# Performance work log

Hardware: AMD Instinct MI355X
Metric: run time of the kernel (lower is better)

## Reference

```python
import jax, jax.numpy as jnp
import numpy as np

NY, NU, NH = 64, 64, 256  # Nhidden=256 -> 128 complex eigen pairs
T, NB = 4096, 32          # horizon, batch


def setup_inputs() -> dict:
    key = jax.random.key(0)
    ks = jax.random.split(key, 9)
    return {
        "y0": jax.random.normal(ks[0], (NB, NY), jnp.float32),
        "U": jax.random.normal(ks[1], (T, NB, NU), jnp.float32),
        "lmbd_cont_real": jax.random.uniform(ks[2], (NH // 2,), jnp.float32),
        "lmbd_cont_imag": jax.random.uniform(ks[3], (NH // 2,), jnp.float32),
        "B": jax.random.normal(ks[4], (NH, NU), jnp.float32) / np.sqrt(NU),
        "W_y2x": jax.random.normal(ks[5], (NH, NY), jnp.float32) / np.sqrt(NY),
        "b_y2x": jax.random.normal(ks[6], (NH,), jnp.float32) * 0.01,
        "W_x2y": jax.random.normal(ks[7], (NY, NH), jnp.float32) / np.sqrt(NH),
        "b_x2y": jax.random.normal(ks[8], (NY,), jnp.float32) * 0.01,
    }


def reference(y0, U, lmbd_cont_real, lmbd_cont_imag, B, W_y2x, b_y2x, W_x2y, b_x2y):
    # where A is the real 2x2-block form of complex eigenvalues
    # lambda = r * exp(i*theta), r = exp(-|re|), theta = (pi/2)*im.
    # Original builds A^n explicitly (O(T^2)); an O(T) scan computes the same math.
    H = B.shape[0] // 2
    Bu = jnp.einsum('tbu,hu->tbh', U, B)          # (T, NB, NH)
    r = jnp.exp(-jnp.abs(lmbd_cont_real))
    theta = (jnp.pi / 2) * lmbd_cont_imag
    lr = r * jnp.cos(theta)                        # Re(lambda), (H,)
    li = r * jnp.sin(theta)                        # Im(lambda), (H,)
    x0 = y0 @ W_y2x.T + b_y2x                      # (NB, NH)
    zr0, zi0 = x0[:, :H], x0[:, H:]
    a, b = Bu[:, :, :H], Bu[:, :, H:]

    def step(carry, inp):
        zr, zi = carry
        ak, bk = inp
        nzr = lr * zr - li * zi + ak
        nzi = li * zr + lr * zi + bk
        return (nzr, nzi), (nzr, nzi)

    _, (Xr, Xi) = jax.lax.scan(step, (zr0, zi0), (a, b))
    X = jnp.concatenate([Xr, Xi], axis=-1)         # (T, NB, NH)
    Y = X @ W_x2y.T + b_x2y                        # (T, NB, NY)
    return Y
```

## Files before the change

kernel.cpp:

```cpp
#include <hip/hip_runtime.h>
#include <math.h>

#define TT   4096
#define NBB  32
#define NUU  64
#define NHH  256
#define HH   128
#define NYY  64
#define LCH  8
#define CCH  512
#define SEGN 16
#define CPS  32

#define PI_HALF 1.5707963267948966f

typedef float  f32x16 __attribute__((ext_vector_type(16)));
typedef __bf16 bf16x8 __attribute__((ext_vector_type(8)));
typedef __bf16 bf16x2 __attribute__((ext_vector_type(2)));
typedef unsigned int uint4v __attribute__((ext_vector_type(4)));

__device__ inline int crow(int r, int lane) { return (r & 3) + 8 * (r >> 2) + 4 * (lane >> 5); }
__device__ inline bf16x8 ldfrag(const unsigned short* p) {
    return __builtin_bit_cast(bf16x8, *(const uint4v*)p);
}

#define CVT(v, H, L) { __bf16 _h = (__bf16)(v); H = _h; L = (__bf16)((v) - (float)_h); }

__device__ inline void lam_f32(float xre, float xim, float& lr, float& li) {
    float th = PI_HALF * xim;
    float rf = (float)exp(-(double)fabsf(xre));
    float cf = (float)cos((double)th);
    float sf = (float)sin((double)th);
    lr = rf * cf; li = rf * sf;
}

__device__ inline int swzU(int row, int so) {
    return row * 128 + ((((so >> 3) ^ row) & 15) << 3) + (so & 7);
}
__device__ inline int swzX(int row, int so) {
    int chv = so >> 3;
    chv = (chv & 32) | ((chv ^ row) & 31);
    return row * 512 + (chv << 3) + (so & 7);
}

__global__ __launch_bounds__(256) void k_prep(
    const float* __restrict__ B, const float* __restrict__ W,
    const float* __restrict__ y0, const float* __restrict__ Wy2x,
    const float* __restrict__ by2x,
    unsigned short* __restrict__ Bph, unsigned short* __restrict__ Bpl,
    unsigned short* __restrict__ Wph, unsigned short* __restrict__ Wpl,
    float2* __restrict__ x0p)
{
    int bx = blockIdx.x, tid = threadIdx.x;
    if (bx < 32) {
        if (tid < HH) {
            int b = bx, ch = tid;
            float xr = by2x[ch], xi = by2x[ch + HH];
            for (int y = 0; y < NYY; ++y) {
                float v = y0[b * NYY + y];
                xr += v * Wy2x[ch * NYY + y];
                xi += v * Wy2x[(ch + HH) * NYY + y];
            }
            x0p[b * HH + ch] = make_float2(xr, xi);
        }
    } else {
        int i = (bx - 32) * 256 + tid;
        float bv = B[i];
        __bf16 bh = (__bf16)bv;
        Bph[i] = __builtin_bit_cast(unsigned short, bh);
        Bpl[i] = __builtin_bit_cast(unsigned short, (__bf16)(bv - (float)bh));
        int y = i >> 8, kidx = i & 255;
        float wv = W[y * NHH + (kidx & 1) * HH + (kidx >> 1)];
        __bf16 wh = (__bf16)wv;
        Wph[i] = __builtin_bit_cast(unsigned short, wh);
        Wpl[i] = __builtin_bit_cast(unsigned short, (__bf16)(wv - (float)wh));
    }
}

__global__ __launch_bounds__(256, 1) void k_pass1(
    const float* __restrict__ U,
    const unsigned short* __restrict__ Bph, const unsigned short* __restrict__ Bpl,
    const float* __restrict__ lre, const float* __restrict__ lim,
    float2* __restrict__ E)
{
    __shared__ __align__(16) unsigned short sU[2][64 * 136];

    const int tid = threadIdx.x, w = tid >> 6, lane = tid & 63;
    const int l31 = lane & 31, kh = lane >> 5;
    const int c = blockIdx.x;
    const int ch = w * 32 + l31;

    float lr, li; lam_f32(lre[ch], lim[ch], lr, li);

    bf16x8 bfh[2][4], bfl[2][4];
#pragma unroll
    for (int nt = 0; nt < 2; ++nt)
#pragma unroll
        for (int kk = 0; kk < 4; ++kk) {
            bfh[nt][kk] = ldfrag(&Bph[(size_t)(nt * HH + ch) * NUU + kk * 16 + kh * 8]);
            bfl[nt][kk] = ldfrag(&Bpl[(size_t)(nt * HH + ch) * NUU + kk * 16 + kh * 8]);
        }

    float zr[16], zi[16];
#pragma unroll
    for (int r = 0; r < 16; ++r) { zr[r] = 0.f; zi[r] = 0.f; }

    const int srow = tid >> 2, sus = (tid & 3) * 16;
    const int sb = srow & 31, stoff = srow >> 5;
    const float* ubase = U + (size_t)sb * NUU + sus;

    float4 f0, f1, f2, f3;
    {
        const float4* sp = (const float4*)(ubase + (size_t)(c * LCH + stoff) * (NBB * NUU));
        f0 = sp[0]; f1 = sp[1]; f2 = sp[2]; f3 = sp[3];
    }

    for (int sub = 0; sub < 4; ++sub) {
        unsigned short* su = &sU[sub & 1][0];
        {
            bf16x8 h0, h1, l0, l1;
            CVT(f0.x, h0[0], l0[0]); CVT(f0.y, h0[1], l0[1]); CVT(f0.z, h0[2], l0[2]); CVT(f0.w, h0[3], l0[3]);
            CVT(f1.x, h0[4], l0[4]); CVT(f1.y, h0[5], l0[5]); CVT(f1.z, h0[6], l0[6]); CVT(f1.w, h0[7], l0[7]);
            CVT(f2.x, h1[0], l1[0]); CVT(f2.y, h1[1], l1[1]); CVT(f2.z, h1[2], l1[2]); CVT(f2.w, h1[3], l1[3]);
            CVT(f3.x, h1[4], l1[4]); CVT(f3.y, h1[5], l1[5]); CVT(f3.z, h1[6], l1[6]); CVT(f3.w, h1[7], l1[7]);
            *(bf16x8*)&su[srow * 136 + sus]          = h0;
            *(bf16x8*)&su[srow * 136 + sus + 8]      = h1;
            *(bf16x8*)&su[srow * 136 + 64 + sus]     = l0;
            *(bf16x8*)&su[srow * 136 + 64 + sus + 8] = l1;
        }
        __syncthreads();

        if (sub < 3) {
            const float4* sp = (const float4*)(ubase + (size_t)(c * LCH + (sub + 1) * 2 + stoff) * (NBB * NUU));
            f0 = sp[0]; f1 = sp[1]; f2 = sp[2]; f3 = sp[3];
        }

        f32x16 acc[2][2];
#pragma unroll
        for (int mt = 0; mt < 2; ++mt)
#pragma unroll
            for (int nt = 0; nt < 2; ++nt)
#pragma unroll
                for (int r = 0; r < 16; ++r) acc[mt][nt][r] = 0.f;

#pragma unroll
        for (int kk = 0; kk < 4; ++kk) {
            bf16x8 a0h = ldfrag(&su[(l31)      * 136 + kk * 16 + kh * 8]);
            bf16x8 a1h = ldfrag(&su[(32 + l31) * 136 + kk * 16 + kh * 8]);
            bf16x8 a0l = ldfrag(&su[(l31)      * 136 + 64 + kk * 16 + kh * 8]);
            bf16x8 a1l = ldfrag(&su[(32 + l31) * 136 + 64 + kk * 16 + kh * 8]);
            acc[0][0] = __builtin_amdgcn_mfma_f32_32x32x16_bf16(a0h, bfh[0][kk], acc[0][0], 0, 0, 0);
            acc[0][1] = __builtin_amdgcn_mfma_f32_32x32x16_bf16(a0h, bfh[1][kk], acc[0][1], 0, 0, 0);
            acc[1][0] = __builtin_amdgcn_mfma_f32_32x32x16_bf16(a1h, bfh[0][kk], acc[1][0], 0, 0, 0);
            acc[1][1] = __builtin_amdgcn_mfma_f32_32x32x16_bf16(a1h, bfh[1][kk], acc[1][1], 0, 0, 0);
            acc[0][0] = __builtin_amdgcn_mfma_f32_32x32x16_bf16(a0l, bfh[0][kk], acc[0][0], 0, 0, 0);
            acc[0][1] = __builtin_amdgcn_mfma_f32_32x32x16_bf16(a0l, bfh[1][kk], acc[0][1], 0, 0, 0);
            acc[1][0] = __builtin_amdgcn_mfma_f32_32x32x16_bf16(a1l, bfh[0][kk], acc[1][0], 0, 0, 0);
            acc[1][1] = __builtin_amdgcn_mfma_f32_32x32x16_bf16(a1l, bfh[1][kk], acc[1][1], 0, 0, 0);
            acc[0][0] = __builtin_amdgcn_mfma_f32_32x32x16_bf16(a0h, bfl[0][kk], acc[0][0], 0, 0, 0);
            acc[0][1] = __builtin_amdgcn_mfma_f32_32x32x16_bf16(a0h, bfl[1][kk], acc[0][1], 0, 0, 0);
            acc[1][0] = __builtin_amdgcn_mfma_f32_32x32x16_bf16(a1h, bfl[0][kk], acc[1][0], 0, 0, 0);
            acc[1][1] = __builtin_amdgcn_mfma_f32_32x32x16_bf16(a1h, bfl[1][kk], acc[1][1], 0, 0, 0);
        }

#pragma unroll
        for (int mt = 0; mt < 2; ++mt)
#pragma unroll
            for (int r = 0; r < 16; ++r) {
                float t0 = fmaf(lr, zr[r], acc[mt][0][r]); t0 = fmaf(-li, zi[r], t0);
                float t1 = fmaf(li, zr[r], acc[mt][1][r]); t1 = fmaf(lr, zi[r], t1);
                zr[r] = t0; zi[r] = t1;
            }
    }

#pragma unroll
    for (int r = 0; r < 16; ++r)
        E[(size_t)c * 4096 + crow(r, lane) * HH + ch] = make_float2(zr[r], zi[r]);
}

__global__ __launch_bounds__(256) void k_cseg(
    const float* __restrict__ lre, const float* __restrict__ lim,
    const float2* __restrict__ E, float2* __restrict__ Esup)
{
    int g = blockIdx.x * 256 + threadIdx.x;
    int chain = g & 4095, seg = g >> 12, ch = chain & 127;
    float lrf, lif; lam_f32(lre[ch], lim[ch], lrf, lif);
    double pr = (double)lrf, pi = (double)lif;
#pragma unroll
    for (int s = 0; s < 3; ++s) { double nr = pr*pr - pi*pi, ni = 2.0*pr*pi; pr = nr; pi = ni; }
    double sr = 0.0, si = 0.0;
#pragma unroll 8
    for (int j = 0; j < CPS; ++j) {
        float2 e = E[((size_t)seg * CPS + j) * 4096 + chain];
        double nr = pr * sr - pi * si + (double)e.x;
        double ni = pi * sr + pr * si + (double)e.y;
        sr = nr; si = ni;
    }
    Esup[(size_t)seg * 4096 + chain] = make_float2((float)sr, (float)si);
}

__global__ __launch_bounds__(256) void k_csup(
    const float* __restrict__ lre, const float* __restrict__ lim,
    const float2* __restrict__ x0p, const float2* __restrict__ Esup,
    float2* __restrict__ CarrySup)
{
    int chain = blockIdx.x * 256 + threadIdx.x;
    int ch = chain & 127;
    float lrf, lif; lam_f32(lre[ch], lim[ch], lrf, lif);
    double pr = (double)lrf, pi = (double)lif;
#pragma unroll
    for (int s = 0; s < 8; ++s) { double nr = pr*pr - pi*pi, ni = 2.0*pr*pi; pr = nr; pi = ni; }
    float2 c0 = x0p[chain];
    double cr = (double)c0.x, ci = (double)c0.y;
#pragma unroll
    for (int s = 0; s < SEGN; ++s) {
        CarrySup[(size_t)s * 4096 + chain] = make_float2((float)cr, (float)ci);
        float2 e = Esup[(size_t)s * 4096 + chain];
        double nr = pr * cr - pi * ci + (double)e.x;
        double ni = pi * cr + pr * ci + (double)e.y;
        cr = nr; ci = ni;
    }
}

__global__ __launch_bounds__(256) void k_cexp(
    const float* __restrict__ lre, const float* __restrict__ lim,
    const float2* __restrict__ E, const float2* __restrict__ CarrySup,
    float2* __restrict__ Carry)
{
    int g = blockIdx.x * 256 + threadIdx.x;
    int chain = g & 4095, seg = g >> 12, ch = chain & 127;
    float lrf, lif; lam_f32(lre[ch], lim[ch], lrf, lif);
    double pr = (double)lrf, pi = (double)lif;
#pragma unroll
    for (int s = 0; s < 3; ++s) { double nr = pr*pr - pi*pi, ni = 2.0*pr*pi; pr = nr; pi = ni; }
    float2 cc = CarrySup[(size_t)seg * 4096 + chain];
    double cr = (double)cc.x, ci = (double)cc.y;
#pragma unroll 8
    for (int j = 0; j < CPS; ++j) {
        size_t idx = ((size_t)seg * CPS + j) * 4096 + chain;
        Carry[idx] = make_float2((float)cr, (float)ci);
        float2 e = E[idx];
        double nr = pr * cr - pi * ci + (double)e.x;
        double ni = pi * cr + pr * ci + (double)e.y;
        cr = nr; ci = ni;
    }
}

__global__ __launch_bounds__(256, 1) void k_pass2(
    const float* __restrict__ U,
    const unsigned short* __restrict__ Bph, const unsigned short* __restrict__ Bpl,
    const unsigned short* __restrict__ Wph, const unsigned short* __restrict__ Wpl,
    const float* __restrict__ lre, const float* __restrict__ lim,
    const float* __restrict__ bx2y,
    const float2* __restrict__ Carry, float* __restrict__ Y)
{
    __shared__ __align__(16) unsigned short sU[64 * 128];
    __shared__ __align__(16) unsigned short sX[64 * 512];

    const int tid = threadIdx.x, w = tid >> 6, lane = tid & 63;
    const int l31 = lane & 31, kh = lane >> 5;
    const int c = blockIdx.x;
    const int ch = w * 32 + l31;
    const int mtile = w & 1, ntile = w >> 1;

    float lr, li; lam_f32(lre[ch], lim[ch], lr, li);
    float ybias = bx2y[ntile * 32 + l31];

    bf16x8 bfh[2][4], bfl[2][4];
#pragma unroll
    for (int nt = 0; nt < 2; ++nt)
#pragma unroll
        for (int kk = 0; kk < 4; ++kk) {
            bfh[nt][kk] = ldfrag(&Bph[(size_t)(nt * HH + ch) * NUU + kk * 16 + kh * 8]);
            bfl[nt][kk] = ldfrag(&Bpl[(size_t)(nt * HH + ch) * NUU + kk * 16 + kh * 8]);
        }

    bf16x8 wfh[16], wfl[16];
#pragma unroll
    for (int kk = 0; kk < 16; ++kk) {
        wfh[kk] = ldfrag(&Wph[(size_t)(ntile * 32 + l31) * NHH + kk * 16 + kh * 8]);
        wfl[kk] = ldfrag(&Wpl[(size_t)(ntile * 32 + l31) * NHH + kk * 16 + kh * 8]);
    }

    float zr[16], zi[16];
#pragma unroll
    for (int r = 0; r < 16; ++r) {
        float2 v = Carry[(size_t)c * 4096 + crow(r, lane) * HH + ch];
        zr[r] = v.x; zi[r] = v.y;
    }

    const int srow = tid >> 2, sus = (tid & 3) * 16;
    const int sb = srow & 31, stoff = srow >> 5;
    const float* ubase = U + (size_t)sb * NUU + sus;

    float4 f0, f1, f2, f3;
    {
        const float4* sp = (const float4*)(ubase + (size_t)(c * LCH + stoff) * (NBB * NUU));
        f0 = sp[0]; f1 = sp[1]; f2 = sp[2]; f3 = sp[3];
    }

    for (int sub = 0; sub < 4; ++sub) {
        {
            bf16x8 h0, h1, l0, l1;
            CVT(f0.x, h0[0], l0[0]); CVT(f0.y, h0[1], l0[1]); CVT(f0.z, h0[2], l0[2]); CVT(f0.w, h0[3], l0[3]);
            CVT(f1.x, h0[4], l0[4]); CVT(f1.y, h0[5], l0[5]); CVT(f1.z, h0[6], l0[6]); CVT(f1.w, h0[7], l0[7]);
            CVT(f2.x, h1[0], l1[0]); CVT(f2.y, h1[1], l1[1]); CVT(f2.z, h1[2], l1[2]); CVT(f2.w, h1[3], l1[3]);
            CVT(f3.x, h1[4], l1[4]); CVT(f3.y, h1[5], l1[5]); CVT(f3.z, h1[6], l1[6]); CVT(f3.w, h1[7], l1[7]);
            *(bf16x8*)&sU[swzU(srow, sus)]          = h0;
            *(bf16x8*)&sU[swzU(srow, sus + 8)]      = h1;
            *(bf16x8*)&sU[swzU(srow, 64 + sus)]     = l0;
            *(bf16x8*)&sU[swzU(srow, 64 + sus + 8)] = l1;
        }

        if (sub > 0) {
            f32x16 ya0, ya1, ya2;
#pragma unroll
            for (int r = 0; r < 16; ++r) { ya0[r] = 0.f; ya1[r] = 0.f; ya2[r] = 0.f; }
#pragma unroll
            for (int kk = 0; kk < 16; ++kk) {
                bf16x8 xah = ldfrag(&sX[swzX(mtile * 32 + l31, kk * 16 + kh * 8)]);
                bf16x8 xal = ldfrag(&sX[swzX(mtile * 32 + l31, 256 + kk * 16 + kh * 8)]);
                ya0 = __builtin_amdgcn_mfma_f32_32x32x16_bf16(xah, wfh[kk], ya0, 0, 0, 0);
                ya1 = __builtin_amdgcn_mfma_f32_32x32x16_bf16(xal, wfh[kk], ya1, 0, 0, 0);
                ya2 = __builtin_amdgcn_mfma_f32_32x32x16_bf16(xah, wfl[kk], ya2, 0, 0, 0);
            }
            int t = c * LCH + (sub - 1) * 2 + mtile;
#pragma unroll
            for (int r = 0; r < 16; ++r)
                Y[((size_t)t * NBB + crow(r, lane)) * NYY + ntile * 32 + l31] =
                    (ya0[r] + ya1[r]) + ya2[r] + ybias;
        }
        __syncthreads();

        if (sub < 3) {
            const float4* sp = (const float4*)(ubase + (size_t)(c * LCH + (sub + 1) * 2 + stoff) * (NBB * NUU));
            f0 = sp[0]; f1 = sp[1]; f2 = sp[2]; f3 = sp[3];
        }

        f32x16 acc[2][2];
#pragma unroll
        for (int mt = 0; mt < 2; ++mt)
#pragma unroll
            for (int nt = 0; nt < 2; ++nt)
#pragma unroll
                for (int r = 0; r < 16; ++r) acc[mt][nt][r] = 0.f;

#pragma unroll
        for (int kk = 0; kk < 4; ++kk) {
            bf16x8 a0h = ldfrag(&sU[swzU(l31,      kk * 16 + kh * 8)]);
            bf16x8 a1h = ldfrag(&sU[swzU(32 + l31, kk * 16 + kh * 8)]);
            bf16x8 a0l = ldfrag(&sU[swzU(l31,      64 + kk * 16 + kh * 8)]);
            bf16x8 a1l = ldfrag(&sU[swzU(32 + l31, 64 + kk * 16 + kh * 8)]);
            acc[0][0] = __builtin_amdgcn_mfma_f32_32x32x16_bf16(a0h, bfh[0][kk], acc[0][0], 0, 0, 0);
            acc[0][1] = __builtin_amdgcn_mfma_f32_32x32x16_bf16(a0h, bfh[1][kk], acc[0][1], 0, 0, 0);
            acc[1][0] = __builtin_amdgcn_mfma_f32_32x32x16_bf16(a1h, bfh[0][kk], acc[1][0], 0, 0, 0);
            acc[1][1] = __builtin_amdgcn_mfma_f32_32x32x16_bf16(a1h, bfh[1][kk], acc[1][1], 0, 0, 0);
            acc[0][0] = __builtin_amdgcn_mfma_f32_32x32x16_bf16(a0l, bfh[0][kk], acc[0][0], 0, 0, 0);
            acc[0][1] = __builtin_amdgcn_mfma_f32_32x32x16_bf16(a0l, bfh[1][kk], acc[0][1], 0, 0, 0);
            acc[1][0] = __builtin_amdgcn_mfma_f32_32x32x16_bf16(a1l, bfh[0][kk], acc[1][0], 0, 0, 0);
            acc[1][1] = __builtin_amdgcn_mfma_f32_32x32x16_bf16(a1l, bfh[1][kk], acc[1][1], 0, 0, 0);
            acc[0][0] = __builtin_amdgcn_mfma_f32_32x32x16_bf16(a0h, bfl[0][kk], acc[0][0], 0, 0, 0);
            acc[0][1] = __builtin_amdgcn_mfma_f32_32x32x16_bf16(a0h, bfl[1][kk], acc[0][1], 0, 0, 0);
            acc[1][0] = __builtin_amdgcn_mfma_f32_32x32x16_bf16(a1h, bfl[0][kk], acc[1][0], 0, 0, 0);
            acc[1][1] = __builtin_amdgcn_mfma_f32_32x32x16_bf16(a1h, bfl[1][kk], acc[1][1], 0, 0, 0);
        }

#pragma unroll
        for (int mt = 0; mt < 2; ++mt)
#pragma unroll
            for (int r = 0; r < 16; ++r) {
                float t0 = fmaf(lr, zr[r], acc[mt][0][r]); t0 = fmaf(-li, zi[r], t0);
                float t1 = fmaf(li, zr[r], acc[mt][1][r]); t1 = fmaf(lr, zi[r], t1);
                zr[r] = t0; zi[r] = t1;
                bf16x2 hv, lv;
                { __bf16 _h = (__bf16)t0; hv[0] = _h; lv[0] = (__bf16)(t0 - (float)_h); }
                { __bf16 _h = (__bf16)t1; hv[1] = _h; lv[1] = (__bf16)(t1 - (float)_h); }
                int row = mt * 32 + crow(r, lane);
                *(bf16x2*)&sX[swzX(row, w * 64 + 2 * l31)]       = hv;
                *(bf16x2*)&sX[swzX(row, 256 + w * 64 + 2 * l31)] = lv;
            }
        __syncthreads();
    }

    {
        f32x16 ya0, ya1, ya2;
#pragma unroll
        for (int r = 0; r < 16; ++r) { ya0[r] = 0.f; ya1[r] = 0.f; ya2[r] = 0.f; }
#pragma unroll
        for (int kk = 0; kk < 16; ++kk) {
            bf16x8 xah = ldfrag(&sX[swzX(mtile * 32 + l31, kk * 16 + kh * 8)]);
            bf16x8 xal = ldfrag(&sX[swzX(mtile * 32 + l31, 256 + kk * 16 + kh * 8)]);
            ya0 = __builtin_amdgcn_mfma_f32_32x32x16_bf16(xah, wfh[kk], ya0, 0, 0, 0);
            ya1 = __builtin_amdgcn_mfma_f32_32x32x16_bf16(xal, wfh[kk], ya1, 0, 0, 0);
            ya2 = __builtin_amdgcn_mfma_f32_32x32x16_bf16(xah, wfl[kk], ya2, 0, 0, 0);
        }
        int t = c * LCH + 3 * 2 + mtile;
#pragma unroll
        for (int r = 0; r < 16; ++r)
            Y[((size_t)t * NBB + crow(r, lane)) * NYY + ntile * 32 + l31] =
                (ya0[r] + ya1[r]) + ya2[r] + ybias;
    }
}

extern "C" void kernel_launch(void* const* d_in, const int* in_sizes, int n_in,
                              void* d_out, int out_size, void* d_ws, size_t ws_size,
                              hipStream_t stream) {
    const float* y0    = (const float*)d_in[0];
    const float* U     = (const float*)d_in[1];
    const float* lre   = (const float*)d_in[2];
    const float* lim   = (const float*)d_in[3];
    const float* B     = (const float*)d_in[4];
    const float* W_y2x = (const float*)d_in[5];
    const float* b_y2x = (const float*)d_in[6];
    const float* W_x2y = (const float*)d_in[7];
    const float* b_x2y = (const float*)d_in[8];
    float* Y = (float*)d_out;

    char* p = (char*)d_ws;
    float2* E        = (float2*)p; p += (size_t)CCH * 4096 * sizeof(float2);
    float2* Carry    = (float2*)p; p += (size_t)CCH * 4096 * sizeof(float2);
    float2* Esup     = (float2*)p; p += (size_t)SEGN * 4096 * sizeof(float2);
    float2* CarrySup = (float2*)p; p += (size_t)SEGN * 4096 * sizeof(float2);
    float2* x0p      = (float2*)p; p += (size_t)4096 * sizeof(float2);
    unsigned short* Bph = (unsigned short*)p; p += 16384 * sizeof(unsigned short);
    unsigned short* Bpl = (unsigned short*)p; p += 16384 * sizeof(unsigned short);
    unsigned short* Wph = (unsigned short*)p; p += 16384 * sizeof(unsigned short);
    unsigned short* Wpl = (unsigned short*)p; p += 16384 * sizeof(unsigned short);

    k_prep <<<dim3(96),  dim3(256), 0, stream>>>(B, W_x2y, y0, W_y2x, b_y2x, Bph, Bpl, Wph, Wpl, x0p);
    k_pass1<<<dim3(CCH), dim3(256), 0, stream>>>(U, Bph, Bpl, lre, lim, E);
    k_cseg <<<dim3(256), dim3(256), 0, stream>>>(lre, lim, E, Esup);
    k_csup <<<dim3(16),  dim3(256), 0, stream>>>(lre, lim, x0p, Esup, CarrySup);
    k_cexp <<<dim3(256), dim3(256), 0, stream>>>(lre, lim, E, CarrySup, Carry);
    k_pass2<<<dim3(CCH), dim3(256), 0, stream>>>(U, Bph, Bpl, Wph, Wpl, lre, lim, b_x2y, Carry, Y);
}
```

Measured before the change: 172.9 us.

## Fold chunk recurrence into lambda-power-weighted B and pre-split U to bf16

Pass1 now folds the 8-step within-chunk recurrence into a single K=512 GEMM, using a B matrix pre-weighted by powers of lambda that is built in the prep kernel. U is converted once to bf16 hi/lo arrays in the prep kernel. Pass1 and pass2 then read MFMA fragments straight from global memory instead of converting and staging through shared memory. This removes the serial recurrence and the repeated fp32-to-bf16 conversion, but adds an extra full write and reread of U (about 32MB of bf16 hi/lo) and a much larger prep grid.

```diff
diff --git a/kernel.cpp b/kernel.cpp
--- a/kernel.cpp
+++ b/kernel.cpp
@@ -34,9 +34,6 @@
     lr = rf * cf; li = rf * sf;
 }
 
-__device__ inline int swzU(int row, int so) {
-    return row * 128 + ((((so >> 3) ^ row) & 15) << 3) + (so & 7);
-}
 __device__ inline int swzX(int row, int so) {
     int chv = so >> 3;
     chv = (chv & 32) | ((chv ^ row) & 31);
@@ -47,8 +44,12 @@
     const float* __restrict__ B, const float* __restrict__ W,
     const float* __restrict__ y0, const float* __restrict__ Wy2x,
     const float* __restrict__ by2x,
+    const float* __restrict__ lre, const float* __restrict__ lim,
+    const float* __restrict__ U,
     unsigned short* __restrict__ Bph, unsigned short* __restrict__ Bpl,
     unsigned short* __restrict__ Wph, unsigned short* __restrict__ Wpl,
+    unsigned short* __restrict__ Bqh, unsigned short* __restrict__ Bql,
+    unsigned short* __restrict__ Uh,  unsigned short* __restrict__ Ul,
     float2* __restrict__ x0p)
 {
     int bx = blockIdx.x, tid = threadIdx.x;
@@ -63,7 +64,7 @@
             }
             x0p[b * HH + ch] = make_float2(xr, xi);
         }
-    } else {
+    } else if (bx < 96) {
         int i = (bx - 32) * 256 + tid;
         float bv = B[i];
         __bf16 bh = (__bf16)bv;
@@ -74,108 +75,81 @@
         __bf16 wh = (__bf16)wv;
         Wph[i] = __builtin_bit_cast(unsigned short, wh);
         Wpl[i] = __builtin_bit_cast(unsigned short, (__bf16)(wv - (float)wh));
-    }
-}
-
-__global__ __launch_bounds__(256, 1) void k_pass1(
-    const float* __restrict__ U,
-    const unsigned short* __restrict__ Bph, const unsigned short* __restrict__ Bpl,
-    const float* __restrict__ lre, const float* __restrict__ lim,
+    } else if (bx < 160) {
+        int e = (bx - 96) * 2048 + tid * 8;
+        int row = e >> 9, col = e & 511;
+        int j = col >> 6, u = col & 63;
+        int ch = (row < HH) ? row : (row - HH);
+        float lrf, lif; lam_f32(lre[ch], lim[ch], lrf, lif);
+        double pr = 1.0, pi_ = 0.0;
+        for (int s = 0; s < 7 - j; ++s) {
+            double nr = pr * (double)lrf - pi_ * (double)lif;
+            double ni = pr * (double)lif + pi_ * (double)lrf;
+            pr = nr; pi_ = ni;
+        }
+        for (int k = 0; k < 8; ++k) {
+            double b0 = (double)B[ch * NUU + u + k];
+            double b1 = (double)B[(ch + HH) * NUU + u + k];
+            float val = (row < HH) ? (float)(pr * b0 - pi_ * b1)
+                                   : (float)(pi_ * b0 + pr * b1);
+            __bf16 vh = (__bf16)val;
+            Bqh[e + k] = __builtin_bit_cast(unsigned short, vh);
+            Bql[e + k] = __builtin_bit_cast(unsigned short, (__bf16)(val - (float)vh));
+        }
+    } else {
+        int e0 = (bx - 160) * 2048 + tid * 8;
+        const float4* s = (const float4*)(U + e0);
+        float4 f0 = s[0], f1 = s[1];
+        bf16x8 h, l;
+        CVT(f0.x, h[0], l[0]); CVT(f0.y, h[1], l[1]); CVT(f0.z, h[2], l[2]); CVT(f0.w, h[3], l[3]);
+        CVT(f1.x, h[4], l[4]); CVT(f1.y, h[5], l[5]); CVT(f1.z, h[6], l[6]); CVT(f1.w, h[7], l[7]);
+        *(bf16x8*)&Uh[e0] = h;
+        *(bf16x8*)&Ul[e0] = l;
+    }
+}
+
+__global__ __launch_bounds__(256) void k_pass1(
+    const unsigned short* __restrict__ Uh, const unsigned short* __restrict__ Ul,
+    const unsigned short* __restrict__ Bqh, const unsigned short* __restrict__ Bql,
     float2* __restrict__ E)
 {
-    __shared__ __align__(16) unsigned short sU[2][64 * 136];
-
     const int tid = threadIdx.x, w = tid >> 6, lane = tid & 63;
     const int l31 = lane & 31, kh = lane >> 5;
     const int c = blockIdx.x;
     const int ch = w * 32 + l31;
 
-    float lr, li; lam_f32(lre[ch], lim[ch], lr, li);
-
-    bf16x8 bfh[2][4], bfl[2][4];
-#pragma unroll
-    for (int nt = 0; nt < 2; ++nt)
-#pragma unroll
-        for (int kk = 0; kk < 4; ++kk) {
-            bfh[nt][kk] = ldfrag(&Bph[(size_t)(nt * HH + ch) * NUU + kk * 16 + kh * 8]);
-            bfl[nt][kk] = ldfrag(&Bpl[(size_t)(nt * HH + ch) * NUU + kk * 16 + kh * 8]);
-        }
-
-    float zr[16], zi[16];
-#pragma unroll
-    for (int r = 0; r < 16; ++r) { zr[r] = 0.f; zi[r] = 0.f; }
-
-    const int srow = tid >> 2, sus = (tid & 3) * 16;
-    const int sb = srow & 31, stoff = srow >> 5;
-    const float* ubase = U + (size_t)sb * NUU + sus;
-
-    float4 f0, f1, f2, f3;
-    {
-        const float4* sp = (const float4*)(ubase + (size_t)(c * LCH + stoff) * (NBB * NUU));
-        f0 = sp[0]; f1 = sp[1]; f2 = sp[2]; f3 = sp[3];
-    }
-
-    for (int sub = 0; sub < 4; ++sub) {
-        unsigned short* su = &sU[sub & 1][0];
-        {
-            bf16x8 h0, h1, l0, l1;
-            CVT(f0.x, h0[0], l0[0]); CVT(f0.y, h0[1], l0[1]); CVT(f0.z, h0[2], l0[2]); CVT(f0.w, h0[3], l0[3]);
-            CVT(f1.x, h0[4], l0[4]); CVT(f1.y, h0[5], l0[5]); CVT(f1.z, h0[6], l0[6]); CVT(f1.w, h0[7], l0[7]);
-            CVT(f2.x, h1[0], l1[0]); CVT(f2.y, h1[1], l1[1]); CVT(f2.z, h1[2], l1[2]); CVT(f2.w, h1[3], l1[3]);
-            CVT(f3.x, h1[4], l1[4]); CVT(f3.y, h1[5], l1[5]); CVT(f3.z, h1[6], l1[6]); CVT(f3.w, h1[7], l1[7]);
-            *(bf16x8*)&su[srow * 136 + sus]          = h0;
-            *(bf16x8*)&su[srow * 136 + sus + 8]      = h1;
-            *(bf16x8*)&su[srow * 136 + 64 + sus]     = l0;
-            *(bf16x8*)&su[srow * 136 + 64 + sus + 8] = l1;
-        }
-        __syncthreads();
-
-        if (sub < 3) {
-            const float4* sp = (const float4*)(ubase + (size_t)(c * LCH + (sub + 1) * 2 + stoff) * (NBB * NUU));
-            f0 = sp[0]; f1 = sp[1]; f2 = sp[2]; f3 = sp[3];
-        }
-
-        f32x16 acc[2][2];
-#pragma unroll
-        for (int mt = 0; mt < 2; ++mt)
-#pragma unroll
-            for (int nt = 0; nt < 2; ++nt)
-#pragma unroll
-                for (int r = 0; r < 16; ++r) acc[mt][nt][r] = 0.f;
-
-#pragma unroll
-        for (int kk = 0; kk < 4; ++kk) {
-            bf16x8 a0h = ldfrag(&su[(l31)      * 136 + kk * 16 + kh * 8]);
-            bf16x8 a1h = ldfrag(&su[(32 + l31) * 136 + kk * 16 + kh * 8]);
-            bf16x8 a0l = ldfrag(&su[(l31)      * 136 + 64 + kk * 16 + kh * 8]);
-            bf16x8 a1l = ldfrag(&su[(32 + l31) * 136 + 64 + kk * 16 + kh * 8]);
-            acc[0][0] = __builtin_amdgcn_mfma_f32_32x32x16_bf16(a0h, bfh[0][kk], acc[0][0], 0, 0, 0);
-            acc[0][1] = __builtin_amdgcn_mfma_f32_32x32x16_bf16(a0h, bfh[1][kk], acc[0][1], 0, 0, 0);
-            acc[1][0] = __builtin_amdgcn_mfma_f32_32x32x16_bf16(a1h, bfh[0][kk], acc[1][0], 0, 0, 0);
-            acc[1][1] = __builtin_amdgcn_mfma_f32_32x32x16_bf16(a1h, bfh[1][kk], acc[1][1], 0, 0, 0);
-            acc[0][0] = __builtin_amdgcn_mfma_f32_32x32x16_bf16(a0l, bfh[0][kk], acc[0][0], 0, 0, 0);
-            acc[0][1] = __builtin_amdgcn_mfma_f32_32x32x16_bf16(a0l, bfh[1][kk], acc[0][1], 0, 0, 0);
-            acc[1][0] = __builtin_amdgcn_mfma_f32_32x32x16_bf16(a1l, bfh[0][kk], acc[1][0], 0, 0, 0);
-            acc[1][1] = __builtin_amdgcn_mfma_f32_32x32x16_bf16(a1l, bfh[1][kk], acc[1][1], 0, 0, 0);
-            acc[0][0] = __builtin_amdgcn_mfma_f32_32x32x16_bf16(a0h, bfl[0][kk], acc[0][0], 0, 0, 0);
-            acc[0][1] = __builtin_amdgcn_mfma_f32_32x32x16_bf16(a0h, bfl[1][kk], acc[0][1], 0, 0, 0);
-            acc[1][0] = __builtin_amdgcn_mfma_f32_32x32x16_bf16(a1h, bfl[0][kk], acc[1][0], 0, 0, 0);
-            acc[1][1] = __builtin_amdgcn_mfma_f32_32x32x16_bf16(a1h, bfl[1][kk], acc[1][1], 0, 0, 0);
-        }
-
-#pragma unroll
-        for (int mt = 0; mt < 2; ++mt)
-#pragma unroll
-            for (int r = 0; r < 16; ++r) {
-                float t0 = fmaf(lr, zr[r], acc[mt][0][r]); t0 = fmaf(-li, zi[r], t0);
-                float t1 = fmaf(li, zr[r], acc[mt][1][r]); t1 = fmaf(lr, zi[r], t1);
-                zr[r] = t0; zi[r] = t1;
-            }
+    const unsigned short* uh = Uh + (size_t)c * (LCH * NBB * NUU) + l31 * 64 + kh * 8;
+    const unsigned short* ul = Ul + (size_t)c * (LCH * NBB * NUU) + l31 * 64 + kh * 8;
+    const unsigned short* b0h = Bqh + (size_t)ch * 512 + kh * 8;
+    const unsigned short* b1h = Bqh + (size_t)(HH + ch) * 512 + kh * 8;
+    const unsigned short* b0l = Bql + (size_t)ch * 512 + kh * 8;
+    const unsigned short* b1l = Bql + (size_t)(HH + ch) * 512 + kh * 8;
+
+    f32x16 acc0, acc1;
+#pragma unroll
+    for (int r = 0; r < 16; ++r) { acc0[r] = 0.f; acc1[r] = 0.f; }
+
+#pragma unroll 4
+    for (int kk = 0; kk < 32; ++kk) {
+        int uoff = (kk >> 2) * 2048 + (kk & 3) * 16;
+        int koff = kk * 16;
+        bf16x8 ah  = ldfrag(uh + uoff);
+        bf16x8 al  = ldfrag(ul + uoff);
+        bf16x8 bh0 = ldfrag(b0h + koff);
+        bf16x8 bh1 = ldfrag(b1h + koff);
+        bf16x8 bl0 = ldfrag(b0l + koff);
+        bf16x8 bl1 = ldfrag(b1l + koff);
+        acc0 = __builtin_amdgcn_mfma_f32_32x32x16_bf16(ah, bh0, acc0, 0, 0, 0);
+        acc1 = __builtin_amdgcn_mfma_f32_32x32x16_bf16(ah, bh1, acc1, 0, 0, 0);
+        acc0 = __builtin_amdgcn_mfma_f32_32x32x16_bf16(al, bh0, acc0, 0, 0, 0);
+        acc1 = __builtin_amdgcn_mfma_f32_32x32x16_bf16(al, bh1, acc1, 0, 0, 0);
+        acc0 = __builtin_amdgcn_mfma_f32_32x32x16_bf16(ah, bl0, acc0, 0, 0, 0);
+        acc1 = __builtin_amdgcn_mfma_f32_32x32x16_bf16(ah, bl1, acc1, 0, 0, 0);
     }
 
 #pragma unroll
     for (int r = 0; r < 16; ++r)
-        E[(size_t)c * 4096 + crow(r, lane) * HH + ch] = make_float2(zr[r], zi[r]);
+        E[(size_t)c * 4096 + crow(r, lane) * HH + ch] = make_float2(acc0[r], acc1[r]);
 }
 
 __global__ __launch_bounds__(256) void k_cseg(
@@ -247,14 +221,13 @@
 }
 
 __global__ __launch_bounds__(256, 1) void k_pass2(
-    const float* __restrict__ U,
+    const unsigned short* __restrict__ Uh, const unsigned short* __restrict__ Ul,
     const unsigned short* __restrict__ Bph, const unsigned short* __restrict__ Bpl,
     const unsigned short* __restrict__ Wph, const unsigned short* __restrict__ Wpl,
     const float* __restrict__ lre, const float* __restrict__ lim,
     const float* __restrict__ bx2y,
     const float2* __restrict__ Carry, float* __restrict__ Y)
 {
-    __shared__ __align__(16) unsigned short sU[64 * 128];
     __shared__ __align__(16) unsigned short sX[64 * 512];
 
     const int tid = threadIdx.x, w = tid >> 6, lane = tid & 63;
@@ -266,14 +239,12 @@
     float lr, li; lam_f32(lre[ch], lim[ch], lr, li);
     float ybias = bx2y[ntile * 32 + l31];
 
-    bf16x8 bfh[2][4], bfl[2][4];
-#pragma unroll
-    for (int nt = 0; nt < 2; ++nt)
-#pragma unroll
-        for (int kk = 0; kk < 4; ++kk) {
-            bfh[nt][kk] = ldfrag(&Bph[(size_t)(nt * HH + ch) * NUU + kk * 16 + kh * 8]);
-            bfl[nt][kk] = ldfrag(&Bpl[(size_t)(nt * HH + ch) * NUU + kk * 16 + kh * 8]);
-        }
+    const unsigned short* uhb = Uh + (size_t)(c * LCH) * (NBB * NUU) + l31 * 64 + kh * 8;
+    const unsigned short* ulb = Ul + (size_t)(c * LCH) * (NBB * NUU) + l31 * 64 + kh * 8;
+    const unsigned short* b0h = Bph + (size_t)ch * NUU + kh * 8;
+    const unsigned short* b1h = Bph + (size_t)(HH + ch) * NUU + kh * 8;
+    const unsigned short* b0l = Bpl + (size_t)ch * NUU + kh * 8;
+    const unsigned short* b1l = Bpl + (size_t)(HH + ch) * NUU + kh * 8;
 
     bf16x8 wfh[16], wfl[16];
 #pragma unroll
@@ -289,29 +260,7 @@
         zr[r] = v.x; zi[r] = v.y;
     }
 
-    const int srow = tid >> 2, sus = (tid & 3) * 16;
-    const int sb = srow & 31, stoff = srow >> 5;
-    const float* ubase = U + (size_t)sb * NUU + sus;
-
-    float4 f0, f1, f2, f3;
-    {
-        const float4* sp = (const float4*)(ubase + (size_t)(c * LCH + stoff) * (NBB * NUU));
-        f0 = sp[0]; f1 = sp[1]; f2 = sp[2]; f3 = sp[3];
-    }
-
     for (int sub = 0; sub < 4; ++sub) {
-        {
-            bf16x8 h0, h1, l0, l1;
-            CVT(f0.x, h0[0], l0[0]); CVT(f0.y, h0[1], l0[1]); CVT(f0.z, h0[2], l0[2]); CVT(f0.w, h0[3], l0[3]);
-            CVT(f1.x, h0[4], l0[4]); CVT(f1.y, h0[5], l0[5]); CVT(f1.z, h0[6], l0[6]); CVT(f1.w, h0[7], l0[7]);
-            CVT(f2.x, h1[0], l1[0]); CVT(f2.y, h1[1], l1[1]); CVT(f2.z, h1[2], l1[2]); CVT(f2.w, h1[3], l1[3]);
-            CVT(f3.x, h1[4], l1[4]); CVT(f3.y, h1[5], l1[5]); CVT(f3.z, h1[6], l1[6]); CVT(f3.w, h1[7], l1[7]);
-            *(bf16x8*)&sU[swzU(srow, sus)]          = h0;
-            *(bf16x8*)&sU[swzU(srow, sus + 8)]      = h1;
-            *(bf16x8*)&sU[swzU(srow, 64 + sus)]     = l0;
-            *(bf16x8*)&sU[swzU(srow, 64 + sus + 8)] = l1;
-        }
-
         if (sub > 0) {
             f32x16 ya0, ya1, ya2;
 #pragma unroll
@@ -332,11 +281,6 @@
         }
         __syncthreads();
 
-        if (sub < 3) {
-            const float4* sp = (const float4*)(ubase + (size_t)(c * LCH + (sub + 1) * 2 + stoff) * (NBB * NUU));
-            f0 = sp[0]; f1 = sp[1]; f2 = sp[2]; f3 = sp[3];
-        }
-
         f32x16 acc[2][2];
 #pragma unroll
         for (int mt = 0; mt < 2; ++mt)
@@ -345,24 +289,29 @@
 #pragma unroll
                 for (int r = 0; r < 16; ++r) acc[mt][nt][r] = 0.f;
 
+        const size_t t0off = (size_t)(sub * 2) * (NBB * NUU);
 #pragma unroll
         for (int kk = 0; kk < 4; ++kk) {
-            bf16x8 a0h = ldfrag(&sU[swzU(l31,      kk * 16 + kh * 8)]);
-            bf16x8 a1h = ldfrag(&sU[swzU(32 + l31, kk * 16 + kh * 8)]);
-            bf16x8 a0l = ldfrag(&sU[swzU(l31,      64 + kk * 16 + kh * 8)]);
-            bf16x8 a1l = ldfrag(&sU[swzU(32 + l31, 64 + kk * 16 + kh * 8)]);
-            acc[0][0] = __builtin_amdgcn_mfma_f32_32x32x16_bf16(a0h, bfh[0][kk], acc[0][0], 0, 0, 0);
-            acc[0][1] = __builtin_amdgcn_mfma_f32_32x32x16_bf16(a0h, bfh[1][kk], acc[0][1], 0, 0, 0);
-            acc[1][0] = __builtin_amdgcn_mfma_f32_32x32x16_bf16(a1h, bfh[0][kk], acc[1][0], 0, 0, 0);
-            acc[1][1] = __builtin_amdgcn_mfma_f32_32x32x16_bf16(a1h, bfh[1][kk], acc[1][1], 0, 0, 0);
-            acc[0][0] = __builtin_amdgcn_mfma_f32_32x32x16_bf16(a0l, bfh[0][kk], acc[0][0], 0, 0, 0);
-            acc[0][1] = __builtin_amdgcn_mfma_f32_32x32x16_bf16(a0l, bfh[1][kk], acc[0][1], 0, 0, 0);
-            acc[1][0] = __builtin_amdgcn_mfma_f32_32x32x16_bf16(a1l, bfh[0][kk], acc[1][0], 0, 0, 0);
-            acc[1][1] = __builtin_amdgcn_mfma_f32_32x32x16_bf16(a1l, bfh[1][kk], acc[1][1], 0, 0, 0);
-            acc[0][0] = __builtin_amdgcn_mfma_f32_32x32x16_bf16(a0h, bfl[0][kk], acc[0][0], 0, 0, 0);
-            acc[0][1] = __builtin_amdgcn_mfma_f32_32x32x16_bf16(a0h, bfl[1][kk], acc[0][1], 0, 0, 0);
-            acc[1][0] = __builtin_amdgcn_mfma_f32_32x32x16_bf16(a1h, bfl[0][kk], acc[1][0], 0, 0, 0);
-            acc[1][1] = __builtin_amdgcn_mfma_f32_32x32x16_bf16(a1h, bfl[1][kk], acc[1][1], 0, 0, 0);
+            bf16x8 a0h = ldfrag(uhb + t0off + kk * 16);
+            bf16x8 a1h = ldfrag(uhb + t0off + (NBB * NUU) + kk * 16);
+            bf16x8 a0l = ldfrag(ulb + t0off + kk * 16);
+            bf16x8 a1l = ldfrag(ulb + t0off + (NBB * NUU) + kk * 16);
+            bf16x8 bh0 = ldfrag(b0h + kk * 16);
+            bf16x8 bh1 = ldfrag(b1h + kk * 16);
+            bf16x8 bl0 = ldfrag(b0l + kk * 16);
+            bf16x8 bl1 = ldfrag(b1l + kk * 16);
+            acc[0][0] = __builtin_amdgcn_mfma_f32_32x32x16_bf16(a0h, bh0, acc[0][0], 0, 0, 0);
+            acc[0][1] = __builtin_amdgcn_mfma_f32_32x32x16_bf16(a0h, bh1, acc[0][1], 0, 0, 0);
+            acc[1][0] = __builtin_amdgcn_mfma_f32_32x32x16_bf16(a1h, bh0, acc[1][0], 0, 0, 0);
+            acc[1][1] = __builtin_amdgcn_mfma_f32_32x32x16_bf16(a1h, bh1, acc[1][1], 0, 0, 0);
+            acc[0][0] = __builtin_amdgcn_mfma_f32_32x32x16_bf16(a0l, bh0, acc[0][0], 0, 0, 0);
+            acc[0][1] = __builtin_amdgcn_mfma_f32_32x32x16_bf16(a0l, bh1, acc[0][1], 0, 0, 0);
+            acc[1][0] = __builtin_amdgcn_mfma_f32_32x32x16_bf16(a1l, bh0, acc[1][0], 0, 0, 0);
+            acc[1][1] = __builtin_amdgcn_mfma_f32_32x32x16_bf16(a1l, bh1, acc[1][1], 0, 0, 0);
+            acc[0][0] = __builtin_amdgcn_mfma_f32_32x32x16_bf16(a0h, bl0, acc[0][0], 0, 0, 0);
+            acc[0][1] = __builtin_amdgcn_mfma_f32_32x32x16_bf16(a0h, bl1, acc[0][1], 0, 0, 0);
+            acc[1][0] = __builtin_amdgcn_mfma_f32_32x32x16_bf16(a1h, bl0, acc[1][0], 0, 0, 0);
+            acc[1][1] = __builtin_amdgcn_mfma_f32_32x32x16_bf16(a1h, bl1, acc[1][1], 0, 0, 0);
         }
 
 #pragma unroll
@@ -426,11 +375,19 @@
     unsigned short* Bpl = (unsigned short*)p; p += 16384 * sizeof(unsigned short);
     unsigned short* Wph = (unsigned short*)p; p += 16384 * sizeof(unsigned short);
     unsigned short* Wpl = (unsigned short*)p; p += 16384 * sizeof(unsigned short);
-
-    k_prep <<<dim3(96),  dim3(256), 0, stream>>>(B, W_x2y, y0, W_y2x, b_y2x, Bph, Bpl, Wph, Wpl, x0p);
-    k_pass1<<<dim3(CCH), dim3(256), 0, stream>>>(U, Bph, Bpl, lre, lim, E);
+    unsigned short* Bqh = (unsigned short*)p; p += (size_t)NHH * 512 * sizeof(unsigned short);
+    unsigned short* Bql = (unsigned short*)p; p += (size_t)NHH * 512 * sizeof(unsigned short);
+    unsigned short* Uh  = (unsigned short*)p; p += (size_t)TT * NBB * NUU * sizeof(unsigned short);
+    unsigned short* Ul  = (unsigned short*)p; p += (size_t)TT * NBB * NUU * sizeof(unsigned short);
+
+    k_prep <<<dim3(4256), dim3(256), 0, stream>>>(B, W_x2y, y0, W_y2x, b_y2x,
+                                                  lre, lim, U,
+                                                  Bph, Bpl, Wph, Wpl,
+                                                  Bqh, Bql, Uh, Ul, x0p);
+    k_pass1<<<dim3(CCH), dim3(256), 0, stream>>>(Uh, Ul, Bqh, Bql, E);
     k_cseg <<<dim3(256), dim3(256), 0, stream>>>(lre, lim, E, Esup);
     k_csup <<<dim3(16),  dim3(256), 0, stream>>>(lre, lim, x0p, Esup, CarrySup);
     k_cexp <<<dim3(256), dim3(256), 0, stream>>>(lre, lim, E, CarrySup, Carry);
-    k_pass2<<<dim3(CCH), dim3(256), 0, stream>>>(U, Bph, Bpl, Wph, Wpl, lre, lim, b_x2y, Carry, Y);
-}
+    k_pass2<<<dim3(CCH), dim3(256), 0, stream>>>(Uh, Ul, Bph, Bpl, Wph, Wpl,
+                                                 lre, lim, b_x2y, Carry, Y);
+}
```

Measured after the change: 217.4 us. +25.7%, slower.

## Restructure pass2 to one timestep per iteration with split-K output reduction

Applied to the files above, without the earlier changes.

Pass2 now advances the recurrence one timestep (32 rows) per iteration instead of two, which halves the sU/sX shared buffers and the accumulator register set. The output projection is split along K across wave pairs, and the two partial sums are combined through a new shared-memory reduction buffer, so each wave holds only 8 W fragments. Launch bounds for pass1 and pass2 are raised to 2 blocks per CU to allow higher occupancy. The cost is twice as many barrier-separated iterations, an extra shared-memory round trip per step, and tighter register limits that may cause spills.

```diff
diff --git a/kernel.cpp b/kernel.cpp
--- a/kernel.cpp
+++ b/kernel.cpp
@@ -34,10 +34,10 @@
     lr = rf * cf; li = rf * sf;
 }
 
-__device__ inline int swzU(int row, int so) {
+__device__ inline int swzU1(int row, int so) {
     return row * 128 + ((((so >> 3) ^ row) & 15) << 3) + (so & 7);
 }
-__device__ inline int swzX(int row, int so) {
+__device__ inline int swzX1(int row, int so) {
     int chv = so >> 3;
     chv = (chv & 32) | ((chv ^ row) & 31);
     return row * 512 + (chv << 3) + (so & 7);
@@ -77,7 +77,7 @@
     }
 }
 
-__global__ __launch_bounds__(256, 1) void k_pass1(
+__global__ __launch_bounds__(256, 2) void k_pass1(
     const float* __restrict__ U,
     const unsigned short* __restrict__ Bph, const unsigned short* __restrict__ Bpl,
     const float* __restrict__ lre, const float* __restrict__ lim,
@@ -246,7 +246,7 @@
     }
 }
 
-__global__ __launch_bounds__(256, 1) void k_pass2(
+__global__ __launch_bounds__(256, 2) void k_pass2(
     const float* __restrict__ U,
     const unsigned short* __restrict__ Bph, const unsigned short* __restrict__ Bpl,
     const unsigned short* __restrict__ Wph, const unsigned short* __restrict__ Wpl,
@@ -254,17 +254,18 @@
     const float* __restrict__ bx2y,
     const float2* __restrict__ Carry, float* __restrict__ Y)
 {
-    __shared__ __align__(16) unsigned short sU[64 * 128];
-    __shared__ __align__(16) unsigned short sX[64 * 512];
+    __shared__ __align__(16) unsigned short sU[32 * 128];
+    __shared__ __align__(16) unsigned short sX[32 * 512];
+    __shared__ float sRed[2][32 * 32];
 
     const int tid = threadIdx.x, w = tid >> 6, lane = tid & 63;
     const int l31 = lane & 31, kh = lane >> 5;
     const int c = blockIdx.x;
     const int ch = w * 32 + l31;
-    const int mtile = w & 1, ntile = w >> 1;
+    const int nt_o = w >> 1, kh2 = w & 1;
 
     float lr, li; lam_f32(lre[ch], lim[ch], lr, li);
-    float ybias = bx2y[ntile * 32 + l31];
+    float ybias = bx2y[nt_o * 32 + l31];
 
     bf16x8 bfh[2][4], bfl[2][4];
 #pragma unroll
@@ -275,11 +276,12 @@
             bfl[nt][kk] = ldfrag(&Bpl[(size_t)(nt * HH + ch) * NUU + kk * 16 + kh * 8]);
         }
 
-    bf16x8 wfh[16], wfl[16];
-#pragma unroll
-    for (int kk = 0; kk < 16; ++kk) {
-        wfh[kk] = ldfrag(&Wph[(size_t)(ntile * 32 + l31) * NHH + kk * 16 + kh * 8]);
-        wfl[kk] = ldfrag(&Wpl[(size_t)(ntile * 32 + l31) * NHH + kk * 16 + kh * 8]);
+    bf16x8 wfh[8], wfl[8];
+#pragma unroll
+    for (int kkl = 0; kkl < 8; ++kkl) {
+        size_t off = (size_t)(nt_o * 32 + l31) * NHH + (kh2 * 8 + kkl) * 16 + kh * 8;
+        wfh[kkl] = ldfrag(&Wph[off]);
+        wfl[kkl] = ldfrag(&Wpl[off]);
     }
 
     float zr[16], zi[16];
@@ -289,116 +291,111 @@
         zr[r] = v.x; zi[r] = v.y;
     }
 
-    const int srow = tid >> 2, sus = (tid & 3) * 16;
-    const int sb = srow & 31, stoff = srow >> 5;
-    const float* ubase = U + (size_t)sb * NUU + sus;
-
-    float4 f0, f1, f2, f3;
+    const int srow = tid >> 3, sus = (tid & 7) * 8;
+    const float* ubase = U + ((size_t)(c * LCH) * NBB + srow) * NUU + sus;
+
+    float4 f0, f1;
+    { const float4* sp = (const float4*)ubase; f0 = sp[0]; f1 = sp[1]; }
+
+    for (int t = 0; t < LCH; ++t) {
+        {
+            bf16x8 h, l;
+            CVT(f0.x, h[0], l[0]); CVT(f0.y, h[1], l[1]); CVT(f0.z, h[2], l[2]); CVT(f0.w, h[3], l[3]);
+            CVT(f1.x, h[4], l[4]); CVT(f1.y, h[5], l[5]); CVT(f1.z, h[6], l[6]); CVT(f1.w, h[7], l[7]);
+            *(bf16x8*)&sU[swzU1(srow, sus)]      = h;
+            *(bf16x8*)&sU[swzU1(srow, 64 + sus)] = l;
+        }
+
+        f32x16 ya0, ya1;
+        if (t > 0) {
+#pragma unroll
+            for (int r = 0; r < 16; ++r) { ya0[r] = 0.f; ya1[r] = 0.f; }
+#pragma unroll
+            for (int kkl = 0; kkl < 8; ++kkl) {
+                int kkg = kh2 * 8 + kkl;
+                bf16x8 xah = ldfrag(&sX[swzX1(l31, kkg * 16 + kh * 8)]);
+                bf16x8 xal = ldfrag(&sX[swzX1(l31, 256 + kkg * 16 + kh * 8)]);
+                ya0 = __builtin_amdgcn_mfma_f32_32x32x16_bf16(xah, wfh[kkl], ya0, 0, 0, 0);
+                ya1 = __builtin_amdgcn_mfma_f32_32x32x16_bf16(xal, wfh[kkl], ya1, 0, 0, 0);
+                ya1 = __builtin_amdgcn_mfma_f32_32x32x16_bf16(xah, wfl[kkl], ya1, 0, 0, 0);
+            }
+            if (kh2 == 1) {
+#pragma unroll
+                for (int r = 0; r < 16; ++r)
+                    sRed[nt_o][crow(r, lane) * 32 + l31] = ya0[r] + ya1[r];
+            }
+        }
+        __syncthreads();
+
+        if (t > 0 && kh2 == 0) {
+            int tt = c * LCH + t - 1;
+#pragma unroll
+            for (int r = 0; r < 16; ++r)
+                Y[((size_t)tt * NBB + crow(r, lane)) * NYY + nt_o * 32 + l31] =
+                    ya0[r] + ya1[r] + sRed[nt_o][crow(r, lane) * 32 + l31] + ybias;
+        }
+
+        if (t < LCH - 1) {
+            const float4* sp = (const float4*)(ubase + (size_t)(t + 1) * (NBB * NUU));
+            f0 = sp[0]; f1 = sp[1];
+        }
+
+        f32x16 acc0, acc1;
+#pragma unroll
+        for (int r = 0; r < 16; ++r) { acc0[r] = 0.f; acc1[r] = 0.f; }
+#pragma unroll
+        for (int kk = 0; kk < 4; ++kk) {
+            bf16x8 a0h = ldfrag(&sU[swzU1(l31, kk * 16 + kh * 8)]);
+            bf16x8 a0l = ldfrag(&sU[swzU1(l31, 64 + kk * 16 + kh * 8)]);
+            acc0 = __builtin_amdgcn_mfma_f32_32x32x16_bf16(a0h, bfh[0][kk], acc0, 0, 0, 0);
+            acc1 = __builtin_amdgcn_mfma_f32_32x32x16_bf16(a0h, bfh[1][kk], acc1, 0, 0, 0);
+            acc0 = __builtin_amdgcn_mfma_f32_32x32x16_bf16(a0l, bfh[0][kk], acc0, 0, 0, 0);
+            acc1 = __builtin_amdgcn_mfma_f32_32x32x16_bf16(a0l, bfh[1][kk], acc1, 0, 0, 0);
+            acc0 = __builtin_amdgcn_mfma_f32_32x32x16_bf16(a0h, bfl[0][kk], acc0, 0, 0, 0);
+            acc1 = __builtin_amdgcn_mfma_f32_32x32x16_bf16(a0h, bfl[1][kk], acc1, 0, 0, 0);
+        }
+
+#pragma unroll
+        for (int r = 0; r < 16; ++r) {
+            float t0 = fmaf(lr, zr[r], acc0[r]); t0 = fmaf(-li, zi[r], t0);
+            float t1 = fmaf(li, zr[r], acc1[r]); t1 = fmaf(lr, zi[r], t1);
+            zr[r] = t0; zi[r] = t1;
+            bf16x2 hv, lv;
+            { __bf16 _h = (__bf16)t0; hv[0] = _h; lv[0] = (__bf16)(t0 - (float)_h); }
+            { __bf16 _h = (__bf16)t1; hv[1] = _h; lv[1] = (__bf16)(t1 - (float)_h); }
+            int row = crow(r, lane);
+            *(bf16x2*)&sX[swzX1(row, w * 64 + 2 * l31)]       = hv;
+            *(bf16x2*)&sX[swzX1(row, 256 + w * 64 + 2 * l31)] = lv;
+        }
+        __syncthreads();
+    }
+
     {
-        const float4* sp = (const float4*)(ubase + (size_t)(c * LCH + stoff) * (NBB * NUU));
-        f0 = sp[0]; f1 = sp[1]; f2 = sp[2]; f3 = sp[3];
-    }
-
-    for (int sub = 0; sub < 4; ++sub) {
-        {
-            bf16x8 h0, h1, l0, l1;
-            CVT(f0.x, h0[0], l0[0]); CVT(f0.y, h0[1], l0[1]); CVT(f0.z, h0[2], l0[2]); CVT(f0.w, h0[3], l0[3]);
-            CVT(f1.x, h0[4], l0[4]); CVT(f1.y, h0[5], l0[5]); CVT(f1.z, h0[6], l0[6]); CVT(f1.w, h0[7], l0[7]);
-            CVT(f2.x, h1[0], l1[0]); CVT(f2.y, h1[1], l1[1]); CVT(f2.z, h1[2], l1[2]); CVT(f2.w, h1[3], l1[3]);
-            CVT(f3.x, h1[4], l1[4]); CVT(f3.y, h1[5], l1[5]); CVT(f3.z, h1[6], l1[6]); CVT(f3.w, h1[7], l1[7]);
-            *(bf16x8*)&sU[swzU(srow, sus)]          = h0;
-            *(bf16x8*)&sU[swzU(srow, sus + 8)]      = h1;
-            *(bf16x8*)&sU[swzU(srow, 64 + sus)]     = l0;
-            *(bf16x8*)&sU[swzU(srow, 64 + sus + 8)] = l1;
-        }
-
-        if (sub > 0) {
-            f32x16 ya0, ya1, ya2;
-#pragma unroll
-            for (int r = 0; r < 16; ++r) { ya0[r] = 0.f; ya1[r] = 0.f; ya2[r] = 0.f; }
-#pragma unroll
-            for (int kk = 0; kk < 16; ++kk) {
-                bf16x8 xah = ldfrag(&sX[swzX(mtile * 32 + l31, kk * 16 + kh * 8)]);
-                bf16x8 xal = ldfrag(&sX[swzX(mtile * 32 + l31, 256 + kk * 16 + kh * 8)]);
-                ya0 = __builtin_amdgcn_mfma_f32_32x32x16_bf16(xah, wfh[kk], ya0, 0, 0, 0);
-                ya1 = __builtin_amdgcn_mfma_f32_32x32x16_bf16(xal, wfh[kk], ya1, 0, 0, 0);
-                ya2 = __builtin_amdgcn_mfma_f32_32x32x16_bf16(xah, wfl[kk], ya2, 0, 0, 0);
-            }
-            int t = c * LCH + (sub - 1) * 2 + mtile;
+        f32x16 ya0, ya1;
+#pragma unroll
+        for (int r = 0; r < 16; ++r) { ya0[r] = 0.f; ya1[r] = 0.f; }
+#pragma unroll
+        for (int kkl = 0; kkl < 8; ++kkl) {
+            int kkg = kh2 * 8 + kkl;
+            bf16x8 xah = ldfrag(&sX[swzX1(l31, kkg * 16 + kh * 8)]);
+            bf16x8 xal = ldfrag(&sX[swzX1(l31, 256 + kkg * 16 + kh * 8)]);
+            ya0 = __builtin_amdgcn_mfma_f32_32x32x16_bf16(xah, wfh[kkl], ya0, 0, 0, 0);
+            ya1 = __builtin_amdgcn_mfma_f32_32x32x16_bf16(xal, wfh[kkl], ya1, 0, 0, 0);
+            ya1 = __builtin_amdgcn_mfma_f32_32x32x16_bf16(xah, wfl[kkl], ya1, 0, 0, 0);
+        }
+        if (kh2 == 1) {
 #pragma unroll
             for (int r = 0; r < 16; ++r)
-                Y[((size_t)t * NBB + crow(r, lane)) * NYY + ntile * 32 + l31] =
-                    (ya0[r] + ya1[r]) + ya2[r] + ybias;
+                sRed[nt_o][crow(r, lane) * 32 + l31] = ya0[r] + ya1[r];
         }
         __syncthreads();
-
-        if (sub < 3) {
-            const float4* sp = (const float4*)(ubase + (size_t)(c * LCH + (sub + 1) * 2 + stoff) * (NBB * NUU));
-            f0 = sp[0]; f1 = sp[1]; f2 = sp[2]; f3 = sp[3];
-        }
-
-        f32x16 acc[2][2];
-#pragma unroll
-        for (int mt = 0; mt < 2; ++mt)
-#pragma unroll
-            for (int nt = 0; nt < 2; ++nt)
-#pragma unroll
-                for (int r = 0; r < 16; ++r) acc[mt][nt][r] = 0.f;
-
-#pragma unroll
-        for (int kk = 0; kk < 4; ++kk) {
-            bf16x8 a0h = ldfrag(&sU[swzU(l31,      kk * 16 + kh * 8)]);
-            bf16x8 a1h = ldfrag(&sU[swzU(32 + l31, kk * 16 + kh * 8)]);
-            bf16x8 a0l = ldfrag(&sU[swzU(l31,      64 + kk * 16 + kh * 8)]);
-            bf16x8 a1l = ldfrag(&sU[swzU(32 + l31, 64 + kk * 16 + kh * 8)]);
-            acc[0][0] = __builtin_amdgcn_mfma_f32_32x32x16_bf16(a0h, bfh[0][kk], acc[0][0], 0, 0, 0);
-            acc[0][1] = __builtin_amdgcn_mfma_f32_32x32x16_bf16(a0h, bfh[1][kk], acc[0][1], 0, 0, 0);
-            acc[1][0] = __builtin_amdgcn_mfma_f32_32x32x16_bf16(a1h, bfh[0][kk], acc[1][0], 0, 0, 0);
-            acc[1][1] = __builtin_amdgcn_mfma_f32_32x32x16_bf16(a1h, bfh[1][kk], acc[1][1], 0, 0, 0);
-            acc[0][0] = __builtin_amdgcn_mfma_f32_32x32x16_bf16(a0l, bfh[0][kk], acc[0][0], 0, 0, 0);
-            acc[0][1] = __builtin_amdgcn_mfma_f32_32x32x16_bf16(a0l, bfh[1][kk], acc[0][1], 0, 0, 0);
-            acc[1][0] = __builtin_amdgcn_mfma_f32_32x32x16_bf16(a1l, bfh[0][kk], acc[1][0], 0, 0, 0);
-            acc[1][1] = __builtin_amdgcn_mfma_f32_32x32x16_bf16(a1l, bfh[1][kk], acc[1][1], 0, 0, 0);
-            acc[0][0] = __builtin_amdgcn_mfma_f32_32x32x16_bf16(a0h, bfl[0][kk], acc[0][0], 0, 0, 0);
-            acc[0][1] = __builtin_amdgcn_mfma_f32_32x32x16_bf16(a0h, bfl[1][kk], acc[0][1], 0, 0, 0);
-            acc[1][0] = __builtin_amdgcn_mfma_f32_32x32x16_bf16(a1h, bfl[0][kk], acc[1][0], 0, 0, 0);
-            acc[1][1] = __builtin_amdgcn_mfma_f32_32x32x16_bf16(a1h, bfl[1][kk], acc[1][1], 0, 0, 0);
-        }
-
-#pragma unroll
-        for (int mt = 0; mt < 2; ++mt)
-#pragma unroll
-            for (int r = 0; r < 16; ++r) {
-                float t0 = fmaf(lr, zr[r], acc[mt][0][r]); t0 = fmaf(-li, zi[r], t0);
-                float t1 = fmaf(li, zr[r], acc[mt][1][r]); t1 = fmaf(lr, zi[r], t1);
-                zr[r] = t0; zi[r] = t1;
-                bf16x2 hv, lv;
-                { __bf16 _h = (__bf16)t0; hv[0] = _h; lv[0] = (__bf16)(t0 - (float)_h); }
-                { __bf16 _h = (__bf16)t1; hv[1] = _h; lv[1] = (__bf16)(t1 - (float)_h); }
-                int row = mt * 32 + crow(r, lane);
-                *(bf16x2*)&sX[swzX(row, w * 64 + 2 * l31)]       = hv;
-                *(bf16x2*)&sX[swzX(row, 256 + w * 64 + 2 * l31)] = lv;
-            }
-        __syncthreads();
-    }
-
-    {
-        f32x16 ya0, ya1, ya2;
-#pragma unroll
-        for (int r = 0; r < 16; ++r) { ya0[r] = 0.f; ya1[r] = 0.f; ya2[r] = 0.f; }
-#pragma unroll
-        for (int kk = 0; kk < 16; ++kk) {
-            bf16x8 xah = ldfrag(&sX[swzX(mtile * 32 + l31, kk * 16 + kh * 8)]);
-            bf16x8 xal = ldfrag(&sX[swzX(mtile * 32 + l31, 256 + kk * 16 + kh * 8)]);
-            ya0 = __builtin_amdgcn_mfma_f32_32x32x16_bf16(xah, wfh[kk], ya0, 0, 0, 0);
-            ya1 = __builtin_amdgcn_mfma_f32_32x32x16_bf16(xal, wfh[kk], ya1, 0, 0, 0);
-            ya2 = __builtin_amdgcn_mfma_f32_32x32x16_bf16(xah, wfl[kk], ya2, 0, 0, 0);
-        }
-        int t = c * LCH + 3 * 2 + mtile;
-#pragma unroll
-        for (int r = 0; r < 16; ++r)
-            Y[((size_t)t * NBB + crow(r, lane)) * NYY + ntile * 32 + l31] =
-                (ya0[r] + ya1[r]) + ya2[r] + ybias;
+        if (kh2 == 0) {
+            int tt = c * LCH + LCH - 1;
+#pragma unroll
+            for (int r = 0; r < 16; ++r)
+                Y[((size_t)tt * NBB + crow(r, lane)) * NYY + nt_o * 32 + l31] =
+                    ya0[r] + ya1[r] + sRed[nt_o][crow(r, lane) * 32 + l31] + ybias;
+        }
     }
 }
 
```

After: 294.4 us. 1.7x slower.
